# Kernel tuning notes

Measured on AMD Instinct MI355X. Metric: run time of the kernel, lower is better.

Reference implementation:

```python
import jax, jax.numpy as jnp
import numpy as np

IN_DIM = 128
OUT_DIM = 128
HEADS = 4
HEAD_DIM = OUT_DIM // HEADS
N_NODES = 50000
N_EDGES = 800000
NEG_SLOPE = 0.2
LN_EPS = 1e-5


def setup_inputs() -> dict:
    key = jax.random.key(0)
    ks = jax.random.split(key, 10)
    x = jax.random.normal(ks[0], (N_NODES, IN_DIM), dtype=jnp.float32)
    edge_index = jax.random.randint(ks[1], (2, N_EDGES), 0, N_NODES, dtype=jnp.int64)
    s = 1.0 / np.sqrt(IN_DIM)
    W_l = jax.random.normal(ks[2], (IN_DIM, HEADS * HEAD_DIM), dtype=jnp.float32) * s
    b_l = jnp.zeros((HEADS * HEAD_DIM,), dtype=jnp.float32)
    W_r = jax.random.normal(ks[3], (IN_DIM, HEADS * HEAD_DIM), dtype=jnp.float32) * s
    b_r = jnp.zeros((HEADS * HEAD_DIM,), dtype=jnp.float32)
    att = jax.random.normal(ks[4], (HEADS, HEAD_DIM), dtype=jnp.float32) * (1.0 / np.sqrt(HEAD_DIM))
    bias = jnp.zeros((HEADS * HEAD_DIM,), dtype=jnp.float32)
    gamma = jnp.ones((OUT_DIM,), dtype=jnp.float32)
    beta = jnp.zeros((OUT_DIM,), dtype=jnp.float32)
    return {"x": x, "edge_index": edge_index, "W_l": W_l, "b_l": b_l,
            "W_r": W_r, "b_r": b_r, "att": att, "bias": bias,
            "gamma": gamma, "beta": beta}


def reference(x, edge_index, W_l, b_l, W_r, b_r, att, bias, gamma, beta):
    N = x.shape[0]
    src, dst = edge_index[0], edge_index[1]
    # GATv2: separate linear transforms for source and target nodes
    xl = (x @ W_l + b_l).reshape(N, HEADS, HEAD_DIM)  # source / message features
    xr = (x @ W_r + b_r).reshape(N, HEADS, HEAD_DIM)  # target features
    # per-edge attention logits: a^T . leaky_relu(xl[src] + xr[dst])  -> [E, H]
    h = jax.nn.leaky_relu(xl[src] + xr[dst], NEG_SLOPE)
    e = jnp.einsum('ehd,hd->eh', h, att)
    # segment softmax over edges grouped by destination node
    m = jax.ops.segment_max(e, dst, num_segments=N)
    m = jnp.where(jnp.isfinite(m), m, 0.0)  # guard empty segments
    ex = jnp.exp(e - m[dst])
    denom = jax.ops.segment_sum(ex, dst, num_segments=N)
    alpha = ex / (denom[dst] + 1e-16)  # [E, H]
    # scatter-add weighted source features (dropout omitted: eval mode)
    out = jax.ops.segment_sum(alpha[:, :, None] * xl[src], dst, num_segments=N)
    out = out.reshape(N, HEADS * HEAD_DIM) + bias
    # residual (in_dim == out_dim) + LayerNorm
    out = out + x
    mu = out.mean(axis=-1, keepdims=True)
    var = ((out - mu) ** 2).mean(axis=-1, keepdims=True)
    return (out - mu) * jax.lax.rsqrt(var + LN_EPS) * gamma + beta
```

## Files before the change

kernel.cpp:

```cpp
#include <hip/hip_runtime.h>
#include <math.h>

#define NEG_SLOPE 0.2f
#define LN_EPS 1e-5f
#define CAP 64
#define HB 8192
#define SLOTS 4608
#define XSTR 136

typedef __attribute__((ext_vector_type(8))) short s8v;
typedef __attribute__((ext_vector_type(8))) unsigned short u8v;
typedef __attribute__((ext_vector_type(4))) float f4v;

__device__ inline unsigned short f2bf(float f) {
    unsigned u = __float_as_uint(f);
    return (unsigned short)((u + 0x7FFFu + ((u >> 16) & 1u)) >> 16);
}
__device__ inline float bf2f(unsigned short h) {
    return __uint_as_float((unsigned)h << 16);
}

__global__ __launch_bounds__(256) void pre_kernel(
    const float* __restrict__ Wl, const float* __restrict__ Wr,
    unsigned short* __restrict__ packL, unsigned short* __restrict__ packR,
    int* __restrict__ gcur, int NBKT) {
    const int bid = blockIdx.x, tid = threadIdx.x;
    if (bid < 2) {
        const float* W = bid ? Wr : Wl;
        unsigned short* pk = bid ? packR : packL;
        for (int idx = tid; idx < 16384; idx += 256) {
            int j = idx & 7;
            int lane = (idx >> 3) & 63;
            int ntt = idx >> 9;
            int t = ntt & 3, nt = ntt >> 2;
            int k = t * 32 + (lane >> 4) * 8 + j;
            int n = nt * 16 + (lane & 15);
            pk[idx] = f2bf(W[k * 128 + n]);
        }
        return;
    }
    if (tid < NBKT) gcur[tid] = 0;
}

__global__ __launch_bounds__(256) void scat_tf_kernel(
    const int* __restrict__ src, const int* __restrict__ dst,
    int* __restrict__ gcur, unsigned* __restrict__ part,
    const float* __restrict__ x,
    const unsigned short* __restrict__ packL, const unsigned short* __restrict__ packR,
    const float* __restrict__ bl, const float* __restrict__ br,
    unsigned short* __restrict__ xl, float* __restrict__ xr,
    int N, int E, int NBKT, int NSC) {
    const int bid = blockIdx.x, tid = threadIdx.x;
    __shared__ __align__(16) char smem[64 * XSTR * 2];

    if (bid < NSC) {
        int* cnt  = (int*)smem;
        int* base = (int*)smem + 256;
        for (int t = tid; t < NBKT; t += 256) cnt[t] = 0;
        __syncthreads();
        const int e0 = bid * HB;
        for (int j = tid; j < HB; j += 256) {
            int e = e0 + j;
            if (e < E) atomicAdd(&cnt[dst[e] >> 8], 1);
        }
        __syncthreads();
        for (int t = tid; t < NBKT; t += 256) {
            base[t] = atomicAdd(&gcur[t], cnt[t]);
            cnt[t] = 0;
        }
        __syncthreads();
        for (int j = tid; j < HB; j += 256) {
            int e = e0 + j;
            if (e < E) {
                int d = dst[e];
                int b = d >> 8;
                int r = atomicAdd(&cnt[b], 1);
                int pos = base[b] + r;
                if (pos < SLOTS)
                    part[(size_t)b * SLOTS + pos] = ((unsigned)d << 16) | (unsigned)src[e];
            }
        }
        return;
    }

    const int rb = bid - NSC;
    unsigned short* xs = (unsigned short*)smem;
    const int blk0 = rb * 64;

    #pragma unroll
    for (int it = 0; it < 8; ++it) {
        int slot = tid + it * 256;
        int row = slot >> 5, c4 = slot & 31;
        int node = blk0 + row;
        float4 v = make_float4(0.f, 0.f, 0.f, 0.f);
        if (node < N) v = *(const float4*)&x[(size_t)node * 128 + 4 * c4];
        ushort4 o;
        o.x = f2bf(v.x); o.y = f2bf(v.y); o.z = f2bf(v.z); o.w = f2bf(v.w);
        *(ushort4*)&xs[row * XSTR + 4 * c4] = o;
    }
    __syncthreads();

    const int wv = tid >> 6, lane = tid & 63;
    const int row = lane & 15, q = lane >> 4;
    const int node0 = blk0 + wv * 16;

    s8v afrag[4];
    #pragma unroll
    for (int t = 0; t < 4; ++t)
        afrag[t] = *(const s8v*)&xs[(wv * 16 + row) * XSTR + t * 32 + q * 8];

    #pragma unroll
    for (int side = 0; side < 2; ++side) {
        const unsigned short* __restrict__ pk = side ? packR : packL;
        const float* __restrict__ bb = side ? br : bl;

        f4v acc[8];
        #pragma unroll
        for (int nt = 0; nt < 8; ++nt) acc[nt] = (f4v){0.f, 0.f, 0.f, 0.f};

        #pragma unroll
        for (int t = 0; t < 4; ++t) {
            #pragma unroll
            for (int nt = 0; nt < 8; ++nt) {
                s8v bfr = *(const s8v*)(pk + (((nt * 4 + t) * 64 + lane) << 3));
                acc[nt] = __builtin_amdgcn_mfma_f32_16x16x32_bf16(afrag[t], bfr, acc[nt], 0, 0, 0);
            }
        }

        #pragma unroll
        for (int nt = 0; nt < 8; ++nt) {
            float bcol = bb[nt * 16 + row];
            #pragma unroll
            for (int r2 = 0; r2 < 4; ++r2) {
                int nd = node0 + q * 4 + r2;
                if (nd < N) {
                    float val = acc[nt][r2] + bcol;
                    if (side) xr[(size_t)nd * 128 + nt * 16 + row] = val;
                    else      xl[(size_t)nd * 128 + nt * 16 + row] = f2bf(val);
                }
            }
        }
    }
}

__global__ __launch_bounds__(256) void fill_kernel(
    const unsigned* __restrict__ part, const int* __restrict__ gcur,
    unsigned short* __restrict__ csr, int* __restrict__ deg, int N) {
    const int b = blockIdx.x, tid = threadIdx.x;
    __shared__ int cur[256];
    cur[tid] = 0;
    __syncthreads();
    int cnt = gcur[b];
    if (cnt > SLOTS) cnt = SLOTS;
    const unsigned* seg = part + (size_t)b * SLOTS;
    for (int i = tid; i < cnt; i += 256) {
        unsigned rec = seg[i];
        int d = rec >> 16;
        int pos = atomicAdd(&cur[d & 255], 1);
        if (pos < CAP) csr[(size_t)d * CAP + pos] = (unsigned short)(rec & 0xFFFFu);
    }
    __syncthreads();
    int node = b * 256 + tid;
    if (node < N) deg[node] = cur[tid];
}

__global__ __launch_bounds__(256) void gat_kernel(
    const int* __restrict__ deg_arr, const unsigned short* __restrict__ csr,
    const unsigned short* __restrict__ xl, const float* __restrict__ xr,
    const float* __restrict__ att, const float* __restrict__ x,
    const float* __restrict__ bias, const float* __restrict__ gamma,
    const float* __restrict__ beta, float* __restrict__ out, int N) {
    const int node = blockIdx.x * 4 + (threadIdx.x >> 6);
    const int lane = threadIdx.x & 63;
    if (node >= N) return;
    const int sub = lane & 15;
    const int eg  = lane >> 4;
    const int f0  = sub * 8;

    float xrf[8], av[8];
    {
        float4 a0 = *(const float4*)&xr[(size_t)node * 128 + f0];
        float4 a1 = *(const float4*)&xr[(size_t)node * 128 + f0 + 4];
        xrf[0] = a0.x; xrf[1] = a0.y; xrf[2] = a0.z; xrf[3] = a0.w;
        xrf[4] = a1.x; xrf[5] = a1.y; xrf[6] = a1.z; xrf[7] = a1.w;
        float4 c0 = *(const float4*)&att[f0];
        float4 c1 = *(const float4*)&att[f0 + 4];
        av[0] = c0.x; av[1] = c0.y; av[2] = c0.z; av[3] = c0.w;
        av[4] = c1.x; av[5] = c1.y; av[6] = c1.z; av[7] = c1.w;
    }

    int dg = deg_arr[node]; if (dg > CAP) dg = CAP;
    const unsigned short* crow = csr + (size_t)node * CAP;

    float den = 0.f;
    float acc[8] = {0.f, 0.f, 0.f, 0.f, 0.f, 0.f, 0.f, 0.f};

    u8v buf0 = {0,0,0,0,0,0,0,0}, buf1 = {0,0,0,0,0,0,0,0};
    if (eg < dg)     buf0 = *(const u8v*)&xl[(size_t)crow[eg] * 128 + f0];
    if (eg + 4 < dg) buf1 = *(const u8v*)&xl[(size_t)crow[eg + 4] * 128 + f0];

    for (int i = eg; i < dg; i += 4) {
        u8v cur = buf0;
        buf0 = buf1;
        if (i + 8 < dg) buf1 = *(const u8v*)&xl[(size_t)crow[i + 8] * 128 + f0];

        float xf[8];
        float p = 0.f;
        #pragma unroll
        for (int j = 0; j < 8; ++j) {
            xf[j] = bf2f(cur[j]);
            float t = xf[j] + xrf[j];
            float h = fmaxf(t, t * NEG_SLOPE);
            p = fmaf(h, av[j], p);
        }
        p += __shfl_xor(p, 1);
        p += __shfl_xor(p, 2);
        float w = __expf(p);
        den += w;
        #pragma unroll
        for (int j = 0; j < 8; ++j) acc[j] = fmaf(w, xf[j], acc[j]);
    }

    den += __shfl_xor(den, 16); den += __shfl_xor(den, 32);
    #pragma unroll
    for (int j = 0; j < 8; ++j) {
        acc[j] += __shfl_xor(acc[j], 16);
        acc[j] += __shfl_xor(acc[j], 32);
    }

    const float inv = 1.0f / (den + 1e-16f);
    float v[8];
    {
        float4 b0 = *(const float4*)&bias[f0];
        float4 b1 = *(const float4*)&bias[f0 + 4];
        float4 r0 = *(const float4*)&x[(size_t)node * 128 + f0];
        float4 r1 = *(const float4*)&x[(size_t)node * 128 + f0 + 4];
        const float bbf[8] = {b0.x, b0.y, b0.z, b0.w, b1.x, b1.y, b1.z, b1.w};
        const float rrf[8] = {r0.x, r0.y, r0.z, r0.w, r1.x, r1.y, r1.z, r1.w};
        #pragma unroll
        for (int j = 0; j < 8; ++j) v[j] = acc[j] * inv + bbf[j] + rrf[j];
    }

    float s = v[0] + v[1] + v[2] + v[3] + v[4] + v[5] + v[6] + v[7];
    s += __shfl_xor(s, 1); s += __shfl_xor(s, 2);
    s += __shfl_xor(s, 4); s += __shfl_xor(s, 8);
    const float mu = s * (1.0f / 128.0f);

    float d[8], vs = 0.f;
    #pragma unroll
    for (int j = 0; j < 8; ++j) { d[j] = v[j] - mu; vs = fmaf(d[j], d[j], vs); }
    vs += __shfl_xor(vs, 1); vs += __shfl_xor(vs, 2);
    vs += __shfl_xor(vs, 4); vs += __shfl_xor(vs, 8);
    const float rstd = rsqrtf(vs * (1.0f / 128.0f) + LN_EPS);

    if (eg == 0) {
        float4 g0 = *(const float4*)&gamma[f0];
        float4 g1 = *(const float4*)&gamma[f0 + 4];
        float4 e0 = *(const float4*)&beta[f0];
        float4 e1 = *(const float4*)&beta[f0 + 4];
        float4 o0, o1;
        o0.x = d[0] * rstd * g0.x + e0.x;  o0.y = d[1] * rstd * g0.y + e0.y;
        o0.z = d[2] * rstd * g0.z + e0.z;  o0.w = d[3] * rstd * g0.w + e0.w;
        o1.x = d[4] * rstd * g1.x + e1.x;  o1.y = d[5] * rstd * g1.y + e1.y;
        o1.z = d[6] * rstd * g1.z + e1.z;  o1.w = d[7] * rstd * g1.w + e1.w;
        *(float4*)&out[(size_t)node * 128 + f0]     = o0;
        *(float4*)&out[(size_t)node * 128 + f0 + 4] = o1;
    }
}

extern "C" void kernel_launch(void* const* d_in, const int* in_sizes, int n_in,
                              void* d_out, int out_size, void* d_ws, size_t ws_size,
                              hipStream_t stream) {
    const float* x     = (const float*)d_in[0];
    const int*   ei    = (const int*)d_in[1];
    const float* Wl    = (const float*)d_in[2];
    const float* bl    = (const float*)d_in[3];
    const float* Wr    = (const float*)d_in[4];
    const float* br    = (const float*)d_in[5];
    const float* att   = (const float*)d_in[6];
    const float* bias  = (const float*)d_in[7];
    const float* gamma = (const float*)d_in[8];
    const float* beta  = (const float*)d_in[9];

    const int N = in_sizes[0] / 128;
    const int E = in_sizes[1] / 2;
    const int* src = ei;
    const int* dst = ei + E;

    const int NBKT = (N + 255) >> 8;
    const int NSC  = (E + HB - 1) / HB;
    const int TBT  = (N + 63) / 64;

    char* w = (char*)d_ws;
    unsigned short* xl    = (unsigned short*)w;  w += (size_t)N * 128 * sizeof(unsigned short);
    float*          xr    = (float*)w;           w += (size_t)N * 128 * sizeof(float);
    unsigned short* packL = (unsigned short*)w;  w += 16384 * sizeof(unsigned short);
    unsigned short* packR = (unsigned short*)w;  w += 16384 * sizeof(unsigned short);
    int*            gcur  = (int*)w;             w += 256 * sizeof(int);
    unsigned*       part  = (unsigned*)w;        w += (size_t)NBKT * SLOTS * sizeof(unsigned);
    unsigned short* csr   = (unsigned short*)w;  w += (size_t)N * CAP * sizeof(unsigned short);
    int*            deg   = (int*)w;             w += (size_t)N * sizeof(int);

    pre_kernel<<<3, 256, 0, stream>>>(Wl, Wr, packL, packR, gcur, NBKT);
    scat_tf_kernel<<<NSC + TBT, 256, 0, stream>>>(
        src, dst, gcur, part, x, packL, packR, bl, br, xl, xr, N, E, NBKT, NSC);
    fill_kernel<<<NBKT, 256, 0, stream>>>(part, gcur, csr, deg, N);
    gat_kernel<<<(N + 3) / 4, 256, 0, stream>>>(
        deg, csr, xl, xr, att, x, bias, gamma, beta, (float*)d_out, N);
}
```

Baseline: 188.9 us.

## Fuse CSR fill into GAT kernel with 64-node buckets in shared memory

Shrinks destination buckets from 256 to 64 nodes and removes the separate fill kernel. Each 1024-thread GAT block now builds its bucket's adjacency lists in shared memory and then processes 64 nodes, 4 per wave, which drops the global CSR and degree writes and reads. xr is also stored as bf16 instead of fp32 to halve its traffic. Risks include lower occupancy from the 1024-thread blocks, serialized per-wave node loops, and bucket overflow or accuracy loss from the smaller SLOTS capacity and bf16 xr.

After: 193.3 us. 2.3% more time.

```diff
diff --git a/kernel.cpp b/kernel.cpp
--- a/kernel.cpp
+++ b/kernel.cpp
@@ -5,7 +5,8 @@
 #define LN_EPS 1e-5f
 #define CAP 64
 #define HB 8192
-#define SLOTS 4608
+#define GBKT 64
+#define SLOTS 1280
 #define XSTR 136
 
 typedef __attribute__((ext_vector_type(8))) short s8v;
@@ -39,7 +40,7 @@
         }
         return;
     }
-    if (tid < NBKT) gcur[tid] = 0;
+    for (int i = tid; i < NBKT; i += 256) gcur[i] = 0;
 }
 
 __global__ __launch_bounds__(256) void scat_tf_kernel(
@@ -48,20 +49,20 @@
     const float* __restrict__ x,
     const unsigned short* __restrict__ packL, const unsigned short* __restrict__ packR,
     const float* __restrict__ bl, const float* __restrict__ br,
-    unsigned short* __restrict__ xl, float* __restrict__ xr,
+    unsigned short* __restrict__ xl, unsigned short* __restrict__ xr,
     int N, int E, int NBKT, int NSC) {
     const int bid = blockIdx.x, tid = threadIdx.x;
     __shared__ __align__(16) char smem[64 * XSTR * 2];
 
     if (bid < NSC) {
         int* cnt  = (int*)smem;
-        int* base = (int*)smem + 256;
+        int* base = (int*)smem + NBKT;
         for (int t = tid; t < NBKT; t += 256) cnt[t] = 0;
         __syncthreads();
         const int e0 = bid * HB;
         for (int j = tid; j < HB; j += 256) {
             int e = e0 + j;
-            if (e < E) atomicAdd(&cnt[dst[e] >> 8], 1);
+            if (e < E) atomicAdd(&cnt[dst[e] >> 6], 1);
         }
         __syncthreads();
         for (int t = tid; t < NBKT; t += 256) {
@@ -73,7 +74,7 @@
             int e = e0 + j;
             if (e < E) {
                 int d = dst[e];
-                int b = d >> 8;
+                int b = d >> 6;
                 int r = atomicAdd(&cnt[b], 1);
                 int pos = base[b] + r;
                 if (pos < SLOTS)
@@ -113,6 +114,7 @@
     for (int side = 0; side < 2; ++side) {
         const unsigned short* __restrict__ pk = side ? packR : packL;
         const float* __restrict__ bb = side ? br : bl;
+        unsigned short* __restrict__ dstp = side ? xr : xl;
 
         f4v acc[8];
         #pragma unroll
@@ -133,138 +135,135 @@
             #pragma unroll
             for (int r2 = 0; r2 < 4; ++r2) {
                 int nd = node0 + q * 4 + r2;
-                if (nd < N) {
-                    float val = acc[nt][r2] + bcol;
-                    if (side) xr[(size_t)nd * 128 + nt * 16 + row] = val;
-                    else      xl[(size_t)nd * 128 + nt * 16 + row] = f2bf(val);
-                }
+                if (nd < N)
+                    dstp[(size_t)nd * 128 + nt * 16 + row] = f2bf(acc[nt][r2] + bcol);
             }
         }
     }
 }
 
-__global__ __launch_bounds__(256) void fill_kernel(
-    const unsigned* __restrict__ part, const int* __restrict__ gcur,
-    unsigned short* __restrict__ csr, int* __restrict__ deg, int N) {
-    const int b = blockIdx.x, tid = threadIdx.x;
-    __shared__ int cur[256];
-    cur[tid] = 0;
-    __syncthreads();
-    int cnt = gcur[b];
-    if (cnt > SLOTS) cnt = SLOTS;
-    const unsigned* seg = part + (size_t)b * SLOTS;
-    for (int i = tid; i < cnt; i += 256) {
-        unsigned rec = seg[i];
-        int d = rec >> 16;
-        int pos = atomicAdd(&cur[d & 255], 1);
-        if (pos < CAP) csr[(size_t)d * CAP + pos] = (unsigned short)(rec & 0xFFFFu);
-    }
-    __syncthreads();
-    int node = b * 256 + tid;
-    if (node < N) deg[node] = cur[tid];
-}
-
-__global__ __launch_bounds__(256) void gat_kernel(
-    const int* __restrict__ deg_arr, const unsigned short* __restrict__ csr,
-    const unsigned short* __restrict__ xl, const float* __restrict__ xr,
+__global__ __launch_bounds__(1024) void gat_kernel(
+    const int* __restrict__ gcur, const unsigned* __restrict__ part,
+    const unsigned short* __restrict__ xl, const unsigned short* __restrict__ xr,
     const float* __restrict__ att, const float* __restrict__ x,
     const float* __restrict__ bias, const float* __restrict__ gamma,
     const float* __restrict__ beta, float* __restrict__ out, int N) {
-    const int node = blockIdx.x * 4 + (threadIdx.x >> 6);
-    const int lane = threadIdx.x & 63;
-    if (node >= N) return;
-    const int sub = lane & 15;
-    const int eg  = lane >> 4;
-    const int f0  = sub * 8;
-
-    float xrf[8], av[8];
+    const int b = blockIdx.x, tid = threadIdx.x;
+    __shared__ unsigned short lcsr[GBKT * CAP];
+    __shared__ int curs[GBKT];
+    if (tid < GBKT) curs[tid] = 0;
+    __syncthreads();
+
+    int cnt = gcur[b]; if (cnt > SLOTS) cnt = SLOTS;
+    const unsigned* seg = part + (size_t)b * SLOTS;
+    for (int i = tid; i < cnt; i += 1024) {
+        unsigned rec = seg[i];
+        int dl = (rec >> 16) & (GBKT - 1);
+        int pos = atomicAdd(&curs[dl], 1);
+        if (pos < CAP) lcsr[dl * CAP + pos] = (unsigned short)(rec & 0xFFFFu);
+    }
+    __syncthreads();
+
+    const int wave = tid >> 6, lane = tid & 63;
+    const int sub = lane & 15, eg = lane >> 4, f0 = sub * 8;
+
+    float av[8];
     {
-        float4 a0 = *(const float4*)&xr[(size_t)node * 128 + f0];
-        float4 a1 = *(const float4*)&xr[(size_t)node * 128 + f0 + 4];
-        xrf[0] = a0.x; xrf[1] = a0.y; xrf[2] = a0.z; xrf[3] = a0.w;
-        xrf[4] = a1.x; xrf[5] = a1.y; xrf[6] = a1.z; xrf[7] = a1.w;
         float4 c0 = *(const float4*)&att[f0];
         float4 c1 = *(const float4*)&att[f0 + 4];
         av[0] = c0.x; av[1] = c0.y; av[2] = c0.z; av[3] = c0.w;
         av[4] = c1.x; av[5] = c1.y; av[6] = c1.z; av[7] = c1.w;
     }
 
-    int dg = deg_arr[node]; if (dg > CAP) dg = CAP;
-    const unsigned short* crow = csr + (size_t)node * CAP;
-
-    float den = 0.f;
-    float acc[8] = {0.f, 0.f, 0.f, 0.f, 0.f, 0.f, 0.f, 0.f};
-
-    u8v buf0 = {0,0,0,0,0,0,0,0}, buf1 = {0,0,0,0,0,0,0,0};
-    if (eg < dg)     buf0 = *(const u8v*)&xl[(size_t)crow[eg] * 128 + f0];
-    if (eg + 4 < dg) buf1 = *(const u8v*)&xl[(size_t)crow[eg + 4] * 128 + f0];
-
-    for (int i = eg; i < dg; i += 4) {
-        u8v cur = buf0;
-        buf0 = buf1;
-        if (i + 8 < dg) buf1 = *(const u8v*)&xl[(size_t)crow[i + 8] * 128 + f0];
-
-        float xf[8];
-        float p = 0.f;
+    for (int k = 0; k < 4; ++k) {
+        const int nl = wave * 4 + k;
+        const int node = b * GBKT + nl;
+        if (node >= N) continue;
+
+        int dg = curs[nl]; if (dg > CAP) dg = CAP;
+        const unsigned short* crow = &lcsr[nl * CAP];
+
+        float xrf[8];
+        {
+            u8v xru = *(const u8v*)&xr[(size_t)node * 128 + f0];
+            #pragma unroll
+            for (int j = 0; j < 8; ++j) xrf[j] = bf2f(xru[j]);
+        }
+
+        float den = 0.f;
+        float acc[8] = {0.f, 0.f, 0.f, 0.f, 0.f, 0.f, 0.f, 0.f};
+
+        u8v buf0 = {0,0,0,0,0,0,0,0}, buf1 = {0,0,0,0,0,0,0,0};
+        if (eg < dg)     buf0 = *(const u8v*)&xl[(size_t)crow[eg] * 128 + f0];
+        if (eg + 4 < dg) buf1 = *(const u8v*)&xl[(size_t)crow[eg + 4] * 128 + f0];
+
+        for (int i = eg; i < dg; i += 4) {
+            u8v curv = buf0;
+            buf0 = buf1;
+            if (i + 8 < dg) buf1 = *(const u8v*)&xl[(size_t)crow[i + 8] * 128 + f0];
+
+            float xf[8];
+            float p = 0.f;
+            #pragma unroll
+            for (int j = 0; j < 8; ++j) {
+                xf[j] = bf2f(curv[j]);
+                float t = xf[j] + xrf[j];
+                float h = fmaxf(t, t * NEG_SLOPE);
+                p = fmaf(h, av[j], p);
+            }
+            p += __shfl_xor(p, 1);
+            p += __shfl_xor(p, 2);
+            float w = __expf(p);
+            den += w;
+            #pragma unroll
+            for (int j = 0; j < 8; ++j) acc[j] = fmaf(w, xf[j], acc[j]);
+        }
+
+        den += __shfl_xor(den, 16); den += __shfl_xor(den, 32);
         #pragma unroll
         for (int j = 0; j < 8; ++j) {
-            xf[j] = bf2f(cur[j]);
-            float t = xf[j] + xrf[j];
-            float h = fmaxf(t, t * NEG_SLOPE);
-            p = fmaf(h, av[j], p);
-        }
-        p += __shfl_xor(p, 1);
-        p += __shfl_xor(p, 2);
-        float w = __expf(p);
-        den += w;
-        #pragma unroll
-        for (int j = 0; j < 8; ++j) acc[j] = fmaf(w, xf[j], acc[j]);
-    }
-
-    den += __shfl_xor(den, 16); den += __shfl_xor(den, 32);
-    #pragma unroll
-    for (int j = 0; j < 8; ++j) {
-        acc[j] += __shfl_xor(acc[j], 16);
-        acc[j] += __shfl_xor(acc[j], 32);
-    }
-
-    const float inv = 1.0f / (den + 1e-16f);
-    float v[8];
-    {
-        float4 b0 = *(const float4*)&bias[f0];
-        float4 b1 = *(const float4*)&bias[f0 + 4];
-        float4 r0 = *(const float4*)&x[(size_t)node * 128 + f0];
-        float4 r1 = *(const float4*)&x[(size_t)node * 128 + f0 + 4];
-        const float bbf[8] = {b0.x, b0.y, b0.z, b0.w, b1.x, b1.y, b1.z, b1.w};
-        const float rrf[8] = {r0.x, r0.y, r0.z, r0.w, r1.x, r1.y, r1.z, r1.w};
-        #pragma unroll
-        for (int j = 0; j < 8; ++j) v[j] = acc[j] * inv + bbf[j] + rrf[j];
-    }
-
-    float s = v[0] + v[1] + v[2] + v[3] + v[4] + v[5] + v[6] + v[7];
-    s += __shfl_xor(s, 1); s += __shfl_xor(s, 2);
-    s += __shfl_xor(s, 4); s += __shfl_xor(s, 8);
-    const float mu = s * (1.0f / 128.0f);
-
-    float d[8], vs = 0.f;
-    #pragma unroll
-    for (int j = 0; j < 8; ++j) { d[j] = v[j] - mu; vs = fmaf(d[j], d[j], vs); }
-    vs += __shfl_xor(vs, 1); vs += __shfl_xor(vs, 2);
-    vs += __shfl_xor(vs, 4); vs += __shfl_xor(vs, 8);
-    const float rstd = rsqrtf(vs * (1.0f / 128.0f) + LN_EPS);
-
-    if (eg == 0) {
-        float4 g0 = *(const float4*)&gamma[f0];
-        float4 g1 = *(const float4*)&gamma[f0 + 4];
-        float4 e0 = *(const float4*)&beta[f0];
-        float4 e1 = *(const float4*)&beta[f0 + 4];
-        float4 o0, o1;
-        o0.x = d[0] * rstd * g0.x + e0.x;  o0.y = d[1] * rstd * g0.y + e0.y;
-        o0.z = d[2] * rstd * g0.z + e0.z;  o0.w = d[3] * rstd * g0.w + e0.w;
-        o1.x = d[4] * rstd * g1.x + e1.x;  o1.y = d[5] * rstd * g1.y + e1.y;
-        o1.z = d[6] * rstd * g1.z + e1.z;  o1.w = d[7] * rstd * g1.w + e1.w;
-        *(float4*)&out[(size_t)node * 128 + f0]     = o0;
-        *(float4*)&out[(size_t)node * 128 + f0 + 4] = o1;
+            acc[j] += __shfl_xor(acc[j], 16);
+            acc[j] += __shfl_xor(acc[j], 32);
+        }
+
+        const float inv = 1.0f / (den + 1e-16f);
+        float v[8];
+        {
+            float4 b0 = *(const float4*)&bias[f0];
+            float4 b1 = *(const float4*)&bias[f0 + 4];
+            float4 r0 = *(const float4*)&x[(size_t)node * 128 + f0];
+            float4 r1 = *(const float4*)&x[(size_t)node * 128 + f0 + 4];
+            const float bbf[8] = {b0.x, b0.y, b0.z, b0.w, b1.x, b1.y, b1.z, b1.w};
+            const float rrf[8] = {r0.x, r0.y, r0.z, r0.w, r1.x, r1.y, r1.z, r1.w};
+            #pragma unroll
+            for (int j = 0; j < 8; ++j) v[j] = acc[j] * inv + bbf[j] + rrf[j];
+        }
+
+        float s = v[0] + v[1] + v[2] + v[3] + v[4] + v[5] + v[6] + v[7];
+        s += __shfl_xor(s, 1); s += __shfl_xor(s, 2);
+        s += __shfl_xor(s, 4); s += __shfl_xor(s, 8);
+        const float mu = s * (1.0f / 128.0f);
+
+        float d[8], vs = 0.f;
+        #pragma unroll
+        for (int j = 0; j < 8; ++j) { d[j] = v[j] - mu; vs = fmaf(d[j], d[j], vs); }
+        vs += __shfl_xor(vs, 1); vs += __shfl_xor(vs, 2);
+        vs += __shfl_xor(vs, 4); vs += __shfl_xor(vs, 8);
+        const float rstd = rsqrtf(vs * (1.0f / 128.0f) + LN_EPS);
+
+        if (eg == 0) {
+            float4 g0 = *(const float4*)&gamma[f0];
+            float4 g1 = *(const float4*)&gamma[f0 + 4];
+            float4 e0 = *(const float4*)&beta[f0];
+            float4 e1 = *(const float4*)&beta[f0 + 4];
+            float4 o0, o1;
+            o0.x = d[0] * rstd * g0.x + e0.x;  o0.y = d[1] * rstd * g0.y + e0.y;
+            o0.z = d[2] * rstd * g0.z + e0.z;  o0.w = d[3] * rstd * g0.w + e0.w;
+            o1.x = d[4] * rstd * g1.x + e1.x;  o1.y = d[5] * rstd * g1.y + e1.y;
+            o1.z = d[6] * rstd * g1.z + e1.z;  o1.w = d[7] * rstd * g1.w + e1.w;
+            *(float4*)&out[(size_t)node * 128 + f0]     = o0;
+            *(float4*)&out[(size_t)node * 128 + f0 + 4] = o1;
+        }
     }
 }
 
@@ -287,24 +286,21 @@
     const int* src = ei;
     const int* dst = ei + E;
 
-    const int NBKT = (N + 255) >> 8;
+    const int NBKT = (N + GBKT - 1) / GBKT;
     const int NSC  = (E + HB - 1) / HB;
     const int TBT  = (N + 63) / 64;
 
     char* w = (char*)d_ws;
     unsigned short* xl    = (unsigned short*)w;  w += (size_t)N * 128 * sizeof(unsigned short);
-    float*          xr    = (float*)w;           w += (size_t)N * 128 * sizeof(float);
+    unsigned short* xr    = (unsigned short*)w;  w += (size_t)N * 128 * sizeof(unsigned short);
     unsigned short* packL = (unsigned short*)w;  w += 16384 * sizeof(unsigned short);
     unsigned short* packR = (unsigned short*)w;  w += 16384 * sizeof(unsigned short);
-    int*            gcur  = (int*)w;             w += 256 * sizeof(int);
+    int*            gcur  = (int*)w;             w += 1024 * sizeof(int);
     unsigned*       part  = (unsigned*)w;        w += (size_t)NBKT * SLOTS * sizeof(unsigned);
-    unsigned short* csr   = (unsigned short*)w;  w += (size_t)N * CAP * sizeof(unsigned short);
-    int*            deg   = (int*)w;             w += (size_t)N * sizeof(int);
 
     pre_kernel<<<3, 256, 0, stream>>>(Wl, Wr, packL, packR, gcur, NBKT);
     scat_tf_kernel<<<NSC + TBT, 256, 0, stream>>>(
         src, dst, gcur, part, x, packL, packR, bl, br, xl, xr, N, E, NBKT, NSC);
-    fill_kernel<<<NBKT, 256, 0, stream>>>(part, gcur, csr, deg, N);
-    gat_kernel<<<(N + 3) / 4, 256, 0, stream>>>(
-        deg, csr, xl, xr, att, x, bias, gamma, beta, (float*)d_out, N);
-}
+    gat_kernel<<<NBKT, 1024, 0, stream>>>(
+        gcur, part, xl, xr, att, x, bias, gamma, beta, (float*)d_out, N);
+}
```
